# Kernel tuning notes

Measured on AMD Instinct MI355X. Metric: run time of the kernel, lower is better.

Reference implementation:

```python
import jax, jax.numpy as jnp
import numpy as np

N_NODES = 50000
N_G_EDGES = 400000
N_LG_EDGES = 600000
N_HEADS = 4
OUT_FEATS = 64
EPS = 0.001


def segment_mean(x, seg_ids, num_segments):
    s = jax.ops.segment_sum(x, seg_ids, num_segments=num_segments)
    cnt = jax.ops.segment_sum(jnp.ones((x.shape[0],), x.dtype), seg_ids, num_segments=num_segments)
    return s / jnp.maximum(cnt, 1.0)[(...,) + (None,) * (x.ndim - 1)]


def setup_inputs() -> dict:
    key = jax.random.key(0)
    ks = jax.random.split(key, 12)
    return {
        'atomic_number': jax.random.randint(ks[0], (N_NODES,), 0, 4),
        'g_src': jax.random.randint(ks[1], (N_G_EDGES,), 0, N_NODES),
        'g_dst': jax.random.randint(ks[2], (N_G_EDGES,), 0, N_NODES),
        'lg_src': jax.random.randint(ks[3], (N_LG_EDGES,), 0, N_G_EDGES),
        'lg_dst': jax.random.randint(ks[4], (N_LG_EDGES,), 0, N_G_EDGES),
        'costheta': jax.random.uniform(ks[5], (N_LG_EDGES,), jnp.float32),
        'dnr': jax.random.uniform(ks[6], (N_LG_EDGES,), jnp.float32),
        'a': jax.random.uniform(ks[7], (N_HEADS,), jnp.float32),
        'b': jax.random.uniform(ks[8], (N_HEADS,), jnp.float32),
        'c': jax.random.uniform(ks[9], (N_HEADS,), jnp.float32),
        'd': jax.random.uniform(ks[10], (N_HEADS,), jnp.float32),
        'value_table': jax.random.normal(ks[11], (4, OUT_FEATS * N_HEADS), jnp.float32),
    }


def reference(atomic_number, g_src, g_dst, lg_src, lg_dst, costheta, dnr, a, b, c, d, value_table):
    # send_k_src: per g-edge atomic numbers of endpoints
    k_src = atomic_number[g_src]  # (E_g,)
    k_dst = atomic_number[g_dst]  # (E_g,)

    # masked symmetry key on line-graph edges (edge pair: lg_src -> lg_dst, g-edge indices)
    ka = k_src[lg_src]
    kc = k_dst[lg_dst]
    kb = k_dst[lg_src]
    peripheral = (ka == kc).astype(jnp.int32)
    central = ((kb == ka) & (kb == kc)).astype(jnp.int32)
    sym_key = peripheral * 2 + central  # (E_lg,), values in {0,1,2,3}

    # value embedding lookup -> (E_lg, F, H)
    asv = value_table[sym_key].reshape(N_LG_EDGES, OUT_FEATS, N_HEADS)

    # angular / radial symmetry per head
    ct = jnp.clip(costheta, -EPS, EPS)
    theta = jnp.arccos(ct)[:, None]  # (E_lg, 1)
    B = b % jnp.pi
    angular = ((jnp.cos(a[None, :] * theta + B[None, :]) + 1.0) / 2.0) ** c[None, :]  # (E_lg, H)
    radial = jnp.exp(-d[None, :] * (dnr[:, None] ** 2))  # (E_lg, H)
    spatial = radial * angular

    sv = asv * spatial[:, None, :]  # (E_lg, F, H)

    # reverse line-graph mean: aggregate lg edges by their (original) source lg-node = g-edge
    w_edge = segment_mean(sv, lg_src, N_G_EDGES)  # (E_g, F, H)
    # reverse graph mean: aggregate g edges by their (original) source node
    w_node = segment_mean(w_edge, g_src, N_NODES)  # (N, F, H)

    return jnp.sum(w_node, axis=-1)  # (N, F)
```

## Files before the change

kernel.cpp:

```cpp
#include <hip/hip_runtime.h>
#include <math.h>

typedef unsigned long long u64;
typedef unsigned int u32;
typedef unsigned short u16;
typedef unsigned char u8;

#define N_NODES    50000
#define N_G_EDGES  400000
#define N_LG_EDGES 600000
#define OUT_FEATS  64
#define EPSV       0.001f
#define PI_F       3.14159265358979323846f
#define FXSCALE    512.0f
#define INV_FXSCALE (1.0f/512.0f)

#define CHUNKS     32
#define RANGES     8
#define GBINS_R    6250
#define GWORDS     1563
#define GSTRIDE    1568
#define LGBINS_R   50000
#define LGWORDS    12500

#define NBUCK      256
#define NPB        196
#define SPB        (NPB*4)
#define CAP        40
#define EPB        2344
#define ENT        (NBUCK*CAP)


__global__ __launch_bounds__(1024, 1) void kA(const int* __restrict__ an,
                                              const int* __restrict__ gsrc,
                                              const int* __restrict__ gdst,
                                              const int* __restrict__ lgsrc,
                                              u8*  __restrict__ kk8,
                                              u32* __restrict__ cg,
                                              u32* __restrict__ clg) {
    __shared__ u32 hist[LGWORDS];
    const int tid = threadIdx.x;
    const int bid = blockIdx.x;
    const int c = bid & (CHUNKS - 1);
    const int r = bid >> 5;
    const int gstart = bid * 1024 + tid;
    const int gstride = CHUNKS * RANGES * 1024;

    for (int g = gstart; g < N_G_EDGES; g += gstride)
        kk8[g] = (u8)(an[gsrc[g]] | (an[gdst[g]] << 4));

    for (int w = tid; w < GWORDS; w += 1024) hist[w] = 0u;
    __syncthreads();
    {
        const int lo = r * GBINS_R;
        const int s0 = c * (N_G_EDGES / CHUNKS);
        const int s1 = s0 + (N_G_EDGES / CHUNKS);
        for (int g = s0 + tid; g < s1; g += 1024) {
            unsigned lb = (unsigned)(gsrc[g] - lo);
            if (lb < (unsigned)GBINS_R)
                atomicAdd(&hist[lb >> 2], 1u << (8 * (lb & 3)));
        }
    }
    __syncthreads();
    for (int w = tid; w < GWORDS; w += 1024) cg[bid * GSTRIDE + w] = hist[w];
    __syncthreads();

    for (int w = tid; w < LGWORDS; w += 1024) hist[w] = 0u;
    __syncthreads();
    {
        const int lo = r * LGBINS_R;
        const int s0 = c * (N_LG_EDGES / CHUNKS);
        const int s1 = s0 + (N_LG_EDGES / CHUNKS);
        for (int e = s0 + tid; e < s1; e += 1024) {
            unsigned lb = (unsigned)(lgsrc[e] - lo);
            if (lb < (unsigned)LGBINS_R)
                atomicAdd(&hist[lb >> 2], 1u << (8 * (lb & 3)));
        }
    }
    __syncthreads();
    for (int w = tid; w < LGWORDS; w += 1024) clg[bid * LGWORDS + w] = hist[w];
}

__global__ void kB(const int* __restrict__ gsrc,
                   const u8*  __restrict__ kk8,
                   const u32* __restrict__ cg,
                   const u32* __restrict__ clg,
                   u64* __restrict__ R,
                   float* __restrict__ inv_g) {
    int g = blockIdx.x * blockDim.x + threadIdx.x;
    if (g >= N_G_EDGES) return;
    {
        int r = g / LGBINS_R, lb = g - r * LGBINS_R;
        int w = lb >> 2, sh = 8 * (lb & 3);
        const u32* base = clg + (size_t)(r * CHUNKS) * LGWORDS + w;
        u32 cnt = 0;
#pragma unroll
        for (int cc = 0; cc < CHUNKS; ++cc) cnt += (base[(size_t)cc * LGWORDS] >> sh) & 0xffu;
        float inv = 1.0f / (float)(cnt < 1u ? 1u : cnt);
        R[g] = ((u64)__float_as_uint(inv) << 32)
             | ((u64)(u32)gsrc[g] << 8)
             | (u64)kk8[g];
    }
    if (g < N_NODES) {
        int r = g / GBINS_R, lb = g - r * GBINS_R;
        int w = lb >> 2, sh = 8 * (lb & 3);
        const u32* base = cg + (size_t)(r * CHUNKS) * GSTRIDE + w;
        u32 cnt = 0;
#pragma unroll
        for (int cc = 0; cc < CHUNKS; ++cc) cnt += (base[(size_t)cc * GSTRIDE] >> sh) & 0xffu;
        inv_g[g] = 1.0f / (float)(cnt < 1u ? 1u : cnt);
    }
}

__global__ __launch_bounds__(1024, 1) void kC1(const int* __restrict__ lgsrc,
                                               const int* __restrict__ lgdst,
                                               const float* __restrict__ costheta,
                                               const float* __restrict__ dnr,
                                               const float* __restrict__ pa,
                                               const float* __restrict__ pb,
                                               const float* __restrict__ pc,
                                               const float* __restrict__ pd,
                                               const u8*  __restrict__ kk8,
                                               const u64* __restrict__ R,
                                               u64* __restrict__ qarr,
                                               u16* __restrict__ sarr,
                                               u32* __restrict__ cnt) {
    __shared__ u32 lcnt[NBUCK];
    const int tid = threadIdx.x;
    const int bid = blockIdx.x;
    if (tid < NBUCK) lcnt[tid] = 0u;
    __syncthreads();

    const int e0 = bid * EPB;
    const int e1 = (e0 + EPB < N_LG_EDGES) ? e0 + EPB : N_LG_EDGES;
    for (int e = e0 + tid; e < e1; e += 1024) {
        u64 r = R[lgsrc[e]];
        int ka = (int)(r & 0xf);
        int kb = (int)((r >> 4) & 0xf);
        int node = (int)((r >> 8) & 0xffff);
        float inv = __uint_as_float((u32)(r >> 32));
        int kd = kk8[lgdst[e]] >> 4;
        int key = ((ka == kd) ? 2 : 0) + ((kb == ka && kb == kd) ? 1 : 0);

        float ct = fminf(fmaxf(costheta[e], -EPSV), EPSV);
        float theta = acosf(ct);
        float dn = dnr[e];
        float dn2 = dn * dn;

        u64 q = 0;
#pragma unroll
        for (int h = 0; h < 4; ++h) {
            float B = fmodf(pb[h], PI_F);
            float ang = __powf((__cosf(pa[h] * theta + B) + 1.0f) * 0.5f, pc[h]);
            float rad = __expf(-pd[h] * dn2);
            float sp = rad * ang * inv;
            q |= (u64)(u32)(sp * FXSCALE + 0.5f) << (16 * h);
        }

        int bucket = node / NPB;
        int slot = (node - bucket * NPB) * 4 + key;
        u32 rank = atomicAdd(&lcnt[bucket], 1u);
        if (rank < CAP) {
            size_t pos = (size_t)bucket * ENT + bid * CAP + rank;
            qarr[pos] = q;
            sarr[pos] = (u16)slot;
        }
    }
    __syncthreads();
    if (tid < NBUCK) {
        u32 v = lcnt[tid];
        cnt[tid * NBUCK + bid] = (v < CAP) ? v : (u32)CAP;
    }
}

__global__ __launch_bounds__(1024, 1) void kC2(const u64* __restrict__ qarr,
                                               const u16* __restrict__ sarr,
                                               const u32* __restrict__ cnt,
                                               const float* __restrict__ inv_g,
                                               const float* __restrict__ VT,
                                               float* __restrict__ out) {
    __shared__ u64 ts[SPB];
    __shared__ u32 c[NBUCK];
    __shared__ float vt_s[1024];
    const int tid = threadIdx.x;
    const int b = blockIdx.x;

    for (int i = tid; i < SPB; i += 1024) ts[i] = 0ull;
    if (tid < NBUCK) c[tid] = cnt[b * NBUCK + tid];
    vt_s[tid] = VT[tid];
    __syncthreads();

    const u64* qb = qarr + (size_t)b * ENT;
    const u16* sb = sarr + (size_t)b * ENT;
    for (int i = tid; i < ENT; i += 1024) {
        int blk = i / CAP;
        int rank = i - blk * CAP;
        if ((u32)rank < c[blk]) {
            u64 q = qb[i];
            int s = sb[i];
            atomicAdd(&ts[s], q);
        }
    }
    __syncthreads();

    const int n0 = b * NPB;
    for (int j = tid; j < NPB * OUT_FEATS; j += 1024) {
        int nl = j >> 6;
        int f = j & 63;
        int n = n0 + nl;
        if (n < N_NODES) {
            float acc = 0.0f;
#pragma unroll
            for (int k = 0; k < 4; ++k) {
                u64 t = ts[nl * 4 + k];
#pragma unroll
                for (int h = 0; h < 4; ++h) {
                    float tv = (float)((u32)(t >> (16 * h)) & 0xffffu);
                    acc += vt_s[k * 256 + f * 4 + h] * tv;
                }
            }
            out[n * OUT_FEATS + f] = acc * INV_FXSCALE * inv_g[n];
        }
    }
}

extern "C" void kernel_launch(void* const* d_in, const int* in_sizes, int n_in,
                              void* d_out, int out_size, void* d_ws, size_t ws_size,
                              hipStream_t stream) {
    const int*   an       = (const int*)d_in[0];
    const int*   gsrc     = (const int*)d_in[1];
    const int*   gdst     = (const int*)d_in[2];
    const int*   lgsrc    = (const int*)d_in[3];
    const int*   lgdst    = (const int*)d_in[4];
    const float* costheta = (const float*)d_in[5];
    const float* dnr      = (const float*)d_in[6];
    const float* pa       = (const float*)d_in[7];
    const float* pb       = (const float*)d_in[8];
    const float* pc       = (const float*)d_in[9];
    const float* pd       = (const float*)d_in[10];
    const float* vt       = (const float*)d_in[11];
    float* out = (float*)d_out;

    char* ws = (char*)d_ws;
    u8*    kk8  = (u8*) (ws + 0);
    u64*   R    = (u64*)(ws + 400000);
    u32*   cg   = (u32*)(ws + 3600000);
    u32*   clg  = (u32*)(ws + 5205632);
    float* invg = (float*)(ws + 18005632);
    u32*   cnt  = (u32*)(ws + 18205632);
    u16*   sarr = (u16*)(ws + 18467776);
    u64*   qarr = (u64*)(ws + 23710656);

    kA<<<dim3(CHUNKS * RANGES), dim3(1024), 0, stream>>>(
        an, gsrc, gdst, lgsrc, kk8, cg, clg);
    kB<<<dim3((N_G_EDGES + 255) / 256), dim3(256), 0, stream>>>(
        gsrc, kk8, cg, clg, R, invg);
    kC1<<<dim3(NBUCK), dim3(1024), 0, stream>>>(
        lgsrc, lgdst, costheta, dnr, pa, pb, pc, pd, kk8, R, qarr, sarr, cnt);
    kC2<<<dim3(NBUCK), dim3(1024), 0, stream>>>(
        qarr, sarr, cnt, invg, vt, out);
}
```

Measured before the change: 59.62 us.

## Fuse histogram and reduce kernels into one range-partitioned count kernel

Replaces the chunked partial-histogram kernel and its separate reduction kernel with one kernel. Each block owns a bin range, scans all source indices, and writes the inverse counts directly, while other blocks compute the packed endpoint atomic numbers. This removes a launch and the large partial-count buffers that had to be written and re-read. The cost is that every histogram block reads the full index array, and kC1 now does separate gathers of gsrc and invlg instead of one packed 64-bit load.

```diff
diff --git a/kernel.cpp b/kernel.cpp
--- a/kernel.cpp
+++ b/kernel.cpp
@@ -15,105 +15,77 @@
 #define FXSCALE    512.0f
 #define INV_FXSCALE (1.0f/512.0f)
 
-#define CHUNKS     32
-#define RANGES     8
-#define GBINS_R    6250
-#define GWORDS     1563
-#define GSTRIDE    1568
-#define LGBINS_R   50000
-#define LGWORDS    12500
-
-#define NBUCK      256
-#define NPB        196
-#define SPB        (NPB*4)
-#define CAP        40
-#define EPB        2344
-#define ENT        (NBUCK*CAP)
-
-
-__global__ __launch_bounds__(1024, 1) void kA(const int* __restrict__ an,
-                                              const int* __restrict__ gsrc,
-                                              const int* __restrict__ gdst,
-                                              const int* __restrict__ lgsrc,
-                                              u8*  __restrict__ kk8,
-                                              u32* __restrict__ cg,
-                                              u32* __restrict__ clg) {
-    __shared__ u32 hist[LGWORDS];
+#define LG_HB     64
+#define LG_BPB    6250
+#define LG_WPB    1563
+#define G_HB      16
+#define G_BPB     3125
+#define G_WPB     782
+#define KB0       80
+#define KB_N      176
+#define KB_GPB    2273
+
+#define NBUCK 256
+#define NPB   196
+#define SPB   (NPB*4)
+#define CAP   40
+#define EPB   2344
+#define ENT   (NBUCK*CAP)
+
+
+__global__ __launch_bounds__(1024) void kA2(const int* __restrict__ an,
+                                            const int* __restrict__ gsrc,
+                                            const int* __restrict__ gdst,
+                                            const int* __restrict__ lgsrc,
+                                            u8*  __restrict__ kk8,
+                                            float* __restrict__ invlg,
+                                            float* __restrict__ invg) {
+    __shared__ u32 hist[LG_WPB];
     const int tid = threadIdx.x;
     const int bid = blockIdx.x;
-    const int c = bid & (CHUNKS - 1);
-    const int r = bid >> 5;
-    const int gstart = bid * 1024 + tid;
-    const int gstride = CHUNKS * RANGES * 1024;
-
-    for (int g = gstart; g < N_G_EDGES; g += gstride)
-        kk8[g] = (u8)(an[gsrc[g]] | (an[gdst[g]] << 4));
-
-    for (int w = tid; w < GWORDS; w += 1024) hist[w] = 0u;
-    __syncthreads();
-    {
-        const int lo = r * GBINS_R;
-        const int s0 = c * (N_G_EDGES / CHUNKS);
-        const int s1 = s0 + (N_G_EDGES / CHUNKS);
-        for (int g = s0 + tid; g < s1; g += 1024) {
+
+    if (bid < LG_HB) {
+        const int lo = bid * LG_BPB;
+        for (int w = tid; w < LG_WPB; w += 1024) hist[w] = 0u;
+        __syncthreads();
+        for (int e = tid; e < N_LG_EDGES; e += 1024) {
+            unsigned lb = (unsigned)(lgsrc[e] - lo);
+            if (lb < (unsigned)LG_BPB)
+                atomicAdd(&hist[lb >> 2], 1u << (8 * (lb & 3)));
+        }
+        __syncthreads();
+        for (int i = tid; i < LG_BPB; i += 1024) {
+            u32 c = (hist[i >> 2] >> (8 * (i & 3))) & 0xffu;
+            invlg[lo + i] = 1.0f / (float)(c < 1u ? 1u : c);
+        }
+    } else if (bid < KB0) {
+        const int lo = (bid - LG_HB) * G_BPB;
+        for (int w = tid; w < G_WPB; w += 1024) hist[w] = 0u;
+        __syncthreads();
+        for (int g = tid; g < N_G_EDGES; g += 1024) {
             unsigned lb = (unsigned)(gsrc[g] - lo);
-            if (lb < (unsigned)GBINS_R)
+            if (lb < (unsigned)G_BPB)
                 atomicAdd(&hist[lb >> 2], 1u << (8 * (lb & 3)));
         }
-    }
-    __syncthreads();
-    for (int w = tid; w < GWORDS; w += 1024) cg[bid * GSTRIDE + w] = hist[w];
-    __syncthreads();
-
-    for (int w = tid; w < LGWORDS; w += 1024) hist[w] = 0u;
-    __syncthreads();
-    {
-        const int lo = r * LGBINS_R;
-        const int s0 = c * (N_LG_EDGES / CHUNKS);
-        const int s1 = s0 + (N_LG_EDGES / CHUNKS);
-        for (int e = s0 + tid; e < s1; e += 1024) {
-            unsigned lb = (unsigned)(lgsrc[e] - lo);
-            if (lb < (unsigned)LGBINS_R)
-                atomicAdd(&hist[lb >> 2], 1u << (8 * (lb & 3)));
-        }
-    }
-    __syncthreads();
-    for (int w = tid; w < LGWORDS; w += 1024) clg[bid * LGWORDS + w] = hist[w];
-}
-
-__global__ void kB(const int* __restrict__ gsrc,
-                   const u8*  __restrict__ kk8,
-                   const u32* __restrict__ cg,
-                   const u32* __restrict__ clg,
-                   u64* __restrict__ R,
-                   float* __restrict__ inv_g) {
-    int g = blockIdx.x * blockDim.x + threadIdx.x;
-    if (g >= N_G_EDGES) return;
-    {
-        int r = g / LGBINS_R, lb = g - r * LGBINS_R;
-        int w = lb >> 2, sh = 8 * (lb & 3);
-        const u32* base = clg + (size_t)(r * CHUNKS) * LGWORDS + w;
-        u32 cnt = 0;
-#pragma unroll
-        for (int cc = 0; cc < CHUNKS; ++cc) cnt += (base[(size_t)cc * LGWORDS] >> sh) & 0xffu;
-        float inv = 1.0f / (float)(cnt < 1u ? 1u : cnt);
-        R[g] = ((u64)__float_as_uint(inv) << 32)
-             | ((u64)(u32)gsrc[g] << 8)
-             | (u64)kk8[g];
-    }
-    if (g < N_NODES) {
-        int r = g / GBINS_R, lb = g - r * GBINS_R;
-        int w = lb >> 2, sh = 8 * (lb & 3);
-        const u32* base = cg + (size_t)(r * CHUNKS) * GSTRIDE + w;
-        u32 cnt = 0;
-#pragma unroll
-        for (int cc = 0; cc < CHUNKS; ++cc) cnt += (base[(size_t)cc * GSTRIDE] >> sh) & 0xffu;
-        inv_g[g] = 1.0f / (float)(cnt < 1u ? 1u : cnt);
+        __syncthreads();
+        for (int i = tid; i < G_BPB; i += 1024) {
+            int n = lo + i;
+            if (n < N_NODES) {
+                u32 c = (hist[i >> 2] >> (8 * (i & 3))) & 0xffu;
+                invg[n] = 1.0f / (float)(c < 1u ? 1u : c);
+            }
+        }
+    } else {
+        const int g0 = (bid - KB0) * KB_GPB;
+        const int g1 = (g0 + KB_GPB < N_G_EDGES) ? g0 + KB_GPB : N_G_EDGES;
+        for (int g = g0 + tid; g < g1; g += 1024)
+            kk8[g] = (u8)(an[gsrc[g]] | (an[gdst[g]] << 4));
     }
 }
 
 __global__ __launch_bounds__(1024, 1) void kC1(const int* __restrict__ lgsrc,
                                                const int* __restrict__ lgdst,
+                                               const int* __restrict__ gsrc,
                                                const float* __restrict__ costheta,
                                                const float* __restrict__ dnr,
                                                const float* __restrict__ pa,
@@ -121,7 +93,7 @@
                                                const float* __restrict__ pc,
                                                const float* __restrict__ pd,
                                                const u8*  __restrict__ kk8,
-                                               const u64* __restrict__ R,
+                                               const float* __restrict__ invlg,
                                                u64* __restrict__ qarr,
                                                u16* __restrict__ sarr,
                                                u32* __restrict__ cnt) {
@@ -134,12 +106,14 @@
     const int e0 = bid * EPB;
     const int e1 = (e0 + EPB < N_LG_EDGES) ? e0 + EPB : N_LG_EDGES;
     for (int e = e0 + tid; e < e1; e += 1024) {
-        u64 r = R[lgsrc[e]];
-        int ka = (int)(r & 0xf);
-        int kb = (int)((r >> 4) & 0xf);
-        int node = (int)((r >> 8) & 0xffff);
-        float inv = __uint_as_float((u32)(r >> 32));
-        int kd = kk8[lgdst[e]] >> 4;
+        int ls = lgsrc[e];
+        int ld = lgdst[e];
+        u32 ks = kk8[ls];
+        int ka = (int)(ks & 0xfu);
+        int kb = (int)(ks >> 4);
+        int kd = kk8[ld] >> 4;
+        int node = gsrc[ls];
+        float inv = invlg[ls];
         int key = ((ka == kd) ? 2 : 0) + ((kb == ka && kb == kd) ? 1 : 0);
 
         float ct = fminf(fmaxf(costheta[e], -EPSV), EPSV);
@@ -242,21 +216,18 @@
     float* out = (float*)d_out;
 
     char* ws = (char*)d_ws;
-    u8*    kk8  = (u8*) (ws + 0);
-    u64*   R    = (u64*)(ws + 400000);
-    u32*   cg   = (u32*)(ws + 3600000);
-    u32*   clg  = (u32*)(ws + 5205632);
-    float* invg = (float*)(ws + 18005632);
-    u32*   cnt  = (u32*)(ws + 18205632);
-    u16*   sarr = (u16*)(ws + 18467776);
-    u64*   qarr = (u64*)(ws + 23710656);
-
-    kA<<<dim3(CHUNKS * RANGES), dim3(1024), 0, stream>>>(
-        an, gsrc, gdst, lgsrc, kk8, cg, clg);
-    kB<<<dim3((N_G_EDGES + 255) / 256), dim3(256), 0, stream>>>(
-        gsrc, kk8, cg, clg, R, invg);
-    kC1<<<dim3(NBUCK), dim3(1024), 0, stream>>>(
-        lgsrc, lgdst, costheta, dnr, pa, pb, pc, pd, kk8, R, qarr, sarr, cnt);
-    kC2<<<dim3(NBUCK), dim3(1024), 0, stream>>>(
+    u8*    kk8   = (u8*)  (ws + 0);
+    float* invlg = (float*)(ws + 400000);
+    float* invg  = (float*)(ws + 2000000);
+    u32*   cnt   = (u32*) (ws + 2200000);
+    u16*   sarr  = (u16*) (ws + 2462144);
+    u64*   qarr  = (u64*) (ws + 7705024);
+
+    kA2<<<dim3(256), dim3(1024), 0, stream>>>(
+        an, gsrc, gdst, lgsrc, kk8, invlg, invg);
+    kC1<<<dim3(256), dim3(1024), 0, stream>>>(
+        lgsrc, lgdst, gsrc, costheta, dnr, pa, pb, pc, pd, kk8, invlg,
+        qarr, sarr, cnt);
+    kC2<<<dim3(256), dim3(1024), 0, stream>>>(
         qarr, sarr, cnt, invg, vt, out);
 }
```

After: 214.3 us. +259.5%, slower.
